# Kernel tuning notes

Measured on AMD Instinct MI355X. Metric: run time of the kernel, lower is better.

The kernel has to match this reference:

```python
import jax, jax.numpy as jnp
import numpy as np
import math

D_MODEL = 1024
NUM_HEADS = 16


def setup_inputs() -> dict:
    key = jax.random.key(0)
    kx, kq, kk, kv, ko = jax.random.split(key, 5)
    std = math.sqrt(2.0 / (D_MODEL + D_MODEL))
    def w(k):
        return (jax.random.truncated_normal(k, -3.0, 3.0, (D_MODEL, D_MODEL), jnp.float32) * std)
    return {
        "x": jax.random.normal(kx, (2, 2048, D_MODEL), jnp.float32),
        "Wq": w(kq),
        "Wk": w(kk),
        "Wv": w(kv),
        "Wo": w(ko),
    }


def reference(x, Wq, Wk, Wv, Wo):
    B, S, D = x.shape
    H = NUM_HEADS
    dh = D // H
    # projections: weight is (d_out, d_in)
    def proj(t, W):
        y = jnp.einsum('bsd,ed->bse', t, W)
        return y.reshape(B, S, H, dh).transpose(0, 2, 1, 3)  # b h s dh
    Q = proj(x, Wq)
    K = proj(x, Wk)
    V = proj(x, Wv)
    scale = 1.0 / math.sqrt(dh)
    logits = jnp.einsum('bhqd,bhkd->bhqk', Q, K) * scale
    mask = jnp.tril(jnp.ones((S, S), dtype=bool))  # causal
    logits = jnp.where(mask, logits, -jnp.inf)
    weights = jax.nn.softmax(logits, axis=-1)
    attn = jnp.einsum('bhqk,bhkd->bhqd', weights, V)
    attn = attn.transpose(0, 2, 1, 3).reshape(B, S, D)
    return jnp.einsum('bsd,ed->bse', attn, Wo)
```

## Files before the change

kernel.cpp:

```cpp
#include <hip/hip_runtime.h>
#include <hip/hip_bf16.h>

typedef __bf16 bf16x8 __attribute__((ext_vector_type(8)));
typedef float  f32x4  __attribute__((ext_vector_type(4)));
typedef float  f32x16 __attribute__((ext_vector_type(16)));
typedef unsigned short u16x8 __attribute__((ext_vector_type(8)));
typedef unsigned short u16x4 __attribute__((ext_vector_type(4)));
typedef unsigned int   u32x4 __attribute__((ext_vector_type(4)));

#define WAITV(N) asm volatile("s_waitcnt vmcnt(" #N ")" ::: "memory")
#define SBAR()   do { __builtin_amdgcn_s_barrier(); asm volatile("" ::: "memory"); } while (0)


__device__ __forceinline__ unsigned short f2bf(float f) {
  return __builtin_bit_cast(unsigned short, (__bf16)f);
}

__device__ __forceinline__ bf16x8 ld8(const unsigned short* p) {
  return __builtin_bit_cast(bf16x8, *reinterpret_cast<const u16x8*>(p));
}

__device__ __forceinline__ unsigned int cvtpk(float a, float b) {
  unsigned int r;
  asm("v_cvt_pk_bf16_f32 %0, %1, %2" : "=v"(r) : "v"(a), "v"(b));
  return r;
}

__device__ __forceinline__ float e2(float x) {
  float r;
  asm("v_exp_f32 %0, %1" : "=v"(r) : "v"(x));
  return r;
}

__device__ __forceinline__ void gload16(const unsigned short* src, unsigned short* lds) {
  __builtin_amdgcn_global_load_lds(
      (const __attribute__((address_space(1))) unsigned int*)src,
      (__attribute__((address_space(3))) unsigned int*)lds,
      16, 0, 0);
}


__global__ __launch_bounds__(256) void cvt_inputs(
    const float* __restrict__ x, const float* __restrict__ Wq,
    const float* __restrict__ Wk, const float* __restrict__ Wv,
    const float* __restrict__ Wo,
    unsigned short* __restrict__ xb, unsigned short* __restrict__ wb) {
  const int NXC = 4194304 / 8;
  const int NWC = 1048576 / 8;
  const int total = NXC + 4 * NWC;
  for (int cid = blockIdx.x * 256 + threadIdx.x; cid < total; cid += gridDim.x * 256) {
    const float* s; unsigned short* d; int off;
    if (cid < NXC) { s = x; d = xb; off = cid * 8; }
    else {
      const int c2 = cid - NXC; const int w = c2 >> 17; const int o2 = c2 & (NWC - 1);
      s = (w == 0) ? Wq : (w == 1) ? Wk : (w == 2) ? Wv : Wo;
      d = wb + (size_t)w * 1048576;
      off = o2 * 8;
    }
    const f32x4 a  = *reinterpret_cast<const f32x4*>(s + off);
    const f32x4 b2 = *reinterpret_cast<const f32x4*>(s + off + 4);
    u16x8 o;
#pragma unroll
    for (int j = 0; j < 4; ++j) { o[j] = f2bf(a[j]); o[j + 4] = f2bf(b2[j]); }
    *reinterpret_cast<u16x8*>(d + off) = o;
  }
}


__global__ __launch_bounds__(256, 2) void gemm_qkv(
    const unsigned short* __restrict__ xb,
    const unsigned short* __restrict__ wb,
    unsigned short* __restrict__ q_s,
    unsigned short* __restrict__ k_s,
    unsigned short* __restrict__ vt_s) {
  __shared__ unsigned short As[2][128 * 64];
  __shared__ unsigned short Bs[2][3][64 * 64];
  const int tid  = threadIdx.x;
  const int lane = tid & 63;
  const int g    = lane >> 4;
  const int lo   = lane & 15;
  const int wid  = tid >> 6;
  const int m0   = blockIdx.y * 128;
  const int n0   = blockIdx.x * 64;
  const int wm   = wid >> 1, wn = wid & 1;

  f32x4 acc[3][4][2] = {};

  auto stage = [&](int buf, int k0) {
#pragma unroll
    for (int i = 0; i < 4; ++i) {
      const int c   = i * 256 + tid;
      const int row = c >> 3, cc = c & 7;
      const int scc = cc ^ (row & 7);
      gload16(xb + (size_t)(m0 + row) * 1024 + k0 + scc * 8, &As[buf][(i * 4 + wid) * 512]);
    }
#pragma unroll
    for (int w = 0; w < 3; ++w)
#pragma unroll
      for (int i = 0; i < 2; ++i) {
        const int c   = i * 256 + tid;
        const int row = c >> 3, cc = c & 7;
        const int scc = cc ^ (row & 7);
        gload16(wb + (size_t)w * 1048576 + (size_t)(n0 + row) * 1024 + k0 + scc * 8,
                &Bs[buf][w][(i * 4 + wid) * 512]);
      }
  };

  stage(0, 0);
  stage(1, 64);
  int cur = 0;
  for (int t = 0; t < 16; ++t) {
    if (t < 15) WAITV(10); else WAITV(0);
    SBAR();
#pragma unroll
    for (int ks = 0; ks < 2; ++ks) {
      const int slot = (ks * 4 + g) ^ (lo & 7);
      bf16x8 af[4];
#pragma unroll
      for (int mi = 0; mi < 4; ++mi)
        af[mi] = ld8(&As[cur][(wm * 64 + mi * 16 + lo) * 64 + slot * 8]);
#pragma unroll
      for (int w = 0; w < 3; ++w) {
        bf16x8 bvf[2];
#pragma unroll
        for (int ni = 0; ni < 2; ++ni)
          bvf[ni] = ld8(&Bs[cur][w][(wn * 32 + ni * 16 + lo) * 64 + slot * 8]);
#pragma unroll
        for (int mi = 0; mi < 4; ++mi)
#pragma unroll
          for (int ni = 0; ni < 2; ++ni)
            acc[w][mi][ni] = __builtin_amdgcn_mfma_f32_16x16x32_bf16(af[mi], bvf[ni], acc[w][mi][ni], 0, 0, 0);
      }
    }
    SBAR();
    if (t + 2 < 16) stage(cur, (t + 2) * 64);
    cur ^= 1;
  }

#pragma unroll
  for (int w = 0; w < 3; ++w) {
    unsigned short* Cv = (w == 0) ? q_s : (w == 1) ? k_s : vt_s;
#pragma unroll
    for (int mi = 0; mi < 4; ++mi) {
#pragma unroll
      for (int ni = 0; ni < 2; ++ni) {
        const int gcol = n0 + wn * 32 + ni * 16 + lo;
        const int h = gcol >> 6, d = gcol & 63;
        if (w == 2) {
          const int s0 = m0 + wm * 64 + mi * 16 + g * 4;
          const int b = s0 >> 11, s = s0 & 2047;
          u16x4 pk;
#pragma unroll
          for (int r = 0; r < 4; ++r) pk[r] = f2bf(acc[w][mi][ni][r]);
          *reinterpret_cast<u16x4*>(&Cv[(((size_t)(b * 16 + h)) * 64 + d) * 2048 + s]) = pk;
        } else {
#pragma unroll
          for (int r = 0; r < 4; ++r) {
            const int grow = m0 + wm * 64 + mi * 16 + g * 4 + r;
            const int b = grow >> 11, s = grow & 2047;
            Cv[(((size_t)(b * 16 + h)) * 2048 + s) * 64 + d] = f2bf(acc[w][mi][ni][r]);
          }
        }
      }
    }
  }
}


__global__ __launch_bounds__(256) void gemm_out(
    const unsigned short* __restrict__ A,
    const unsigned short* __restrict__ wb,
    float* __restrict__ out) {
  const unsigned short* W = wb + (size_t)3 * 1048576;
  __shared__ unsigned short As[2][128 * 64];
  __shared__ unsigned short Bs[2][64 * 64];
  const int tid  = threadIdx.x;
  const int lane = tid & 63;
  const int g    = lane >> 4;
  const int lo   = lane & 15;
  const int wid  = tid >> 6;
  const int m0   = blockIdx.y * 128;
  const int n0   = blockIdx.x * 64;
  const int wm   = wid >> 1, wn = wid & 1;

  f32x4 acc[4][2] = {};

  auto stage = [&](int buf, int k0) {
#pragma unroll
    for (int i = 0; i < 4; ++i) {
      const int c   = i * 256 + tid;
      const int row = c >> 3, cc = c & 7;
      const int scc = cc ^ (row & 7);
      gload16(A + (size_t)(m0 + row) * 1024 + k0 + scc * 8, &As[buf][(i * 4 + wid) * 512]);
    }
#pragma unroll
    for (int i = 0; i < 2; ++i) {
      const int c   = i * 256 + tid;
      const int row = c >> 3, cc = c & 7;
      const int scc = cc ^ (row & 7);
      gload16(W + (size_t)(n0 + row) * 1024 + k0 + scc * 8, &Bs[buf][(i * 4 + wid) * 512]);
    }
  };

  stage(0, 0);
  stage(1, 64);
  int cur = 0;
  for (int t = 0; t < 16; ++t) {
    if (t < 15) WAITV(6); else WAITV(0);
    SBAR();
#pragma unroll
    for (int ks = 0; ks < 2; ++ks) {
      const int slot = (ks * 4 + g) ^ (lo & 7);
      bf16x8 af[4], bvf[2];
#pragma unroll
      for (int mi = 0; mi < 4; ++mi)
        af[mi] = ld8(&As[cur][(wm * 64 + mi * 16 + lo) * 64 + slot * 8]);
#pragma unroll
      for (int ni = 0; ni < 2; ++ni)
        bvf[ni] = ld8(&Bs[cur][(wn * 32 + ni * 16 + lo) * 64 + slot * 8]);
#pragma unroll
      for (int mi = 0; mi < 4; ++mi)
#pragma unroll
        for (int ni = 0; ni < 2; ++ni)
          acc[mi][ni] = __builtin_amdgcn_mfma_f32_16x16x32_bf16(af[mi], bvf[ni], acc[mi][ni], 0, 0, 0);
    }
    SBAR();
    if (t + 2 < 16) stage(cur, (t + 2) * 64);
    cur ^= 1;
  }

#pragma unroll
  for (int mi = 0; mi < 4; ++mi)
#pragma unroll
    for (int ni = 0; ni < 2; ++ni) {
      const int gcol = n0 + wn * 32 + ni * 16 + lo;
#pragma unroll
      for (int r = 0; r < 4; ++r) {
        const int grow = m0 + wm * 64 + mi * 16 + g * 4 + r;
        out[(size_t)grow * 1024 + gcol] = acc[mi][ni][r];
      }
    }
}


__global__ __launch_bounds__(512, 4) void attn_fwd(
    const unsigned short* __restrict__ Q,
    const unsigned short* __restrict__ K,
    const unsigned short* __restrict__ Vt,
    unsigned short* __restrict__ O) {
  __shared__ unsigned short Kl[2][128 * 64];
  __shared__ unsigned short Vl[2][2][64 * 64];
  const int tid  = threadIdx.x;
  const int lane = tid & 63;
  const int wid  = tid >> 6;
  const int qs   = wid & 3;
  const int kh   = wid >> 2;
  const int q31  = lane & 31;
  const int hi   = lane >> 5;
  const int bi   = blockIdx.x;
  const int bh   = bi & 31;
  const int j    = (bi < 256) ? (15 - (bi >> 5)) : ((bi - 256) >> 5);
  const int b    = bh >> 4, h = bh & 15;

  const unsigned short* Qb = Q  + (size_t)bh * 2048 * 64;
  const unsigned short* Kb = K  + (size_t)bh * 2048 * 64;
  const unsigned short* Vb = Vt + (size_t)bh * 64 * 2048;
  const float SC = 0.125f * 1.4426950408889634f;

  auto stage = [&](int buf, int t) {
#pragma unroll
    for (int i = 0; i < 2; ++i) {
      const int c   = i * 512 + tid;
      const int row = c >> 3, cc = c & 7;
      const int scc = cc ^ (row & 7);
      gload16(Kb + (size_t)(t * 128 + row) * 64 + scc * 8, &Kl[buf][(i * 8 + wid) * 512]);
    }
#pragma unroll
    for (int i = 0; i < 2; ++i) {
      const int d  = tid >> 3, cc = tid & 7;
      const int scc = cc ^ (d & 7);
      gload16(Vb + (size_t)d * 2048 + t * 128 + i * 64 + scc * 8, &Vl[buf][i][wid * 512]);
    }
  };

  const int R  = j + 1;
  const int qv = j * 128 + qs * 32 + q31;

  bf16x8 qf[4];
#pragma unroll
  for (int ds = 0; ds < 4; ++ds) {
    bf16x8 tq = ld8(Qb + (size_t)qv * 64 + ds * 16 + hi * 8);
#pragma unroll
    for (int jx = 0; jx < 8; ++jx) tq[jx] = (__bf16)((float)tq[jx] * SC);
    qf[ds] = tq;
  }

  f32x16 oacc[2] = {};
  float m = -1.0e30f;
  float l = 0.f;

  stage(0, 0);
  int buf = 0;

  for (int t = 0; t < R; ++t) {
    SBAR();
    if (t + 1 < R) { stage(buf ^ 1, t + 1); WAITV(4); }
    else WAITV(0);
    SBAR();

    const bool lastt = (t == j);
    const bool skipw = lastt && (kh == 1) && (qs < 2);
    if (!skipw) {
      f32x16 sv[2];
      __builtin_amdgcn_s_setprio(1);
#pragma unroll
      for (int kt2 = 0; kt2 < 2; ++kt2) {
        const int row = kh * 64 + kt2 * 32 + q31;
        f32x16 a = {};
#pragma unroll
        for (int ds = 0; ds < 4; ++ds) {
          bf16x8 kf = ld8(&Kl[buf][row * 64 + ((ds * 2 + hi) ^ (row & 7)) * 8]);
          a = __builtin_amdgcn_mfma_f32_32x32x16_bf16(kf, qf[ds], a, 0, 0, 0);
        }
        sv[kt2] = a;
      }
      __builtin_amdgcn_s_setprio(0);

      const bool domask = lastt && !(kh == 0 && qs >= 2);
      float t0 = -1.0e30f, t1 = -1.0e30f, t2 = -1.0e30f, t3 = -1.0e30f;
      if (domask) {
#pragma unroll
        for (int kt2 = 0; kt2 < 2; ++kt2)
#pragma unroll
          for (int r = 0; r < 16; ++r) {
            float v = sv[kt2][r];
            const int key = t * 128 + kh * 64 + kt2 * 32 + (r & 3) + 8 * (r >> 2) + 4 * hi;
            if (key > qv) v = -INFINITY;
            sv[kt2][r] = v;
            if ((r & 3) == 0) t0 = fmaxf(t0, v);
            else if ((r & 3) == 1) t1 = fmaxf(t1, v);
            else if ((r & 3) == 2) t2 = fmaxf(t2, v);
            else t3 = fmaxf(t3, v);
          }
      } else {
#pragma unroll
        for (int kt2 = 0; kt2 < 2; ++kt2)
#pragma unroll
          for (int r = 0; r < 16; ++r) {
            const float v = sv[kt2][r];
            if ((r & 3) == 0) t0 = fmaxf(t0, v);
            else if ((r & 3) == 1) t1 = fmaxf(t1, v);
            else if ((r & 3) == 2) t2 = fmaxf(t2, v);
            else t3 = fmaxf(t3, v);
          }
      }
      const float tmax = fmaxf(fmaxf(t0, t1), fmaxf(t2, t3));

      if (!__all(tmax <= m + 8.f)) {
        float rmax = fmaxf(tmax, __shfl_xor(tmax, 32));
        const float mn   = fmaxf(m, rmax);
        const float corr = e2(m - mn);
        l *= corr;
#pragma unroll
        for (int dt = 0; dt < 2; ++dt)
#pragma unroll
          for (int r = 0; r < 16; ++r) oacc[dt][r] *= corr;
        m = mn;
      }

      float p0 = 0.f, p1 = 0.f, p2 = 0.f, p3 = 0.f;
#pragma unroll
      for (int kt2 = 0; kt2 < 2; ++kt2)
#pragma unroll
        for (int r = 0; r < 16; ++r) {
          const float p = e2(sv[kt2][r] - m);
          sv[kt2][r] = p;
          if ((r & 3) == 0) p0 += p;
          else if ((r & 3) == 1) p1 += p;
          else if ((r & 3) == 2) p2 += p;
          else p3 += p;
        }
      l += (p0 + p1) + (p2 + p3);

      unsigned int pw[4][4];
#pragma unroll
      for (int ks = 0; ks < 4; ++ks) {
        const int kt2 = ks >> 1, Rr = (ks & 1) * 8;
        unsigned int a0 = cvtpk(sv[kt2][Rr + 0], sv[kt2][Rr + 1]);
        unsigned int c0 = cvtpk(sv[kt2][Rr + 4], sv[kt2][Rr + 5]);
        unsigned int a1 = cvtpk(sv[kt2][Rr + 2], sv[kt2][Rr + 3]);
        unsigned int c1 = cvtpk(sv[kt2][Rr + 6], sv[kt2][Rr + 7]);
        asm("v_permlane32_swap_b32 %0, %1" : "+v"(a0), "+v"(c0));
        asm("v_permlane32_swap_b32 %0, %1" : "+v"(a1), "+v"(c1));
        pw[ks][0] = a0; pw[ks][1] = a1; pw[ks][2] = c0; pw[ks][3] = c1;
      }

      __builtin_amdgcn_s_setprio(1);
#pragma unroll
      for (int dt = 0; dt < 2; ++dt) {
        const int dl = dt * 32 + q31;
#pragma unroll
        for (int ks = 0; ks < 4; ++ks) {
          bf16x8 vfr = ld8(&Vl[buf][kh][dl * 64 + ((ks * 2 + hi) ^ (dl & 7)) * 8]);
          u32x4 t4 = {pw[ks][0], pw[ks][1], pw[ks][2], pw[ks][3]};
          bf16x8 pb = __builtin_bit_cast(bf16x8, t4);
          oacc[dt] = __builtin_amdgcn_mfma_f32_32x32x16_bf16(vfr, pb, oacc[dt], 0, 0, 0);
        }
      }
      __builtin_amdgcn_s_setprio(0);
    }

    buf ^= 1;
  }

  SBAR();
  float* VlF = (float*)&Vl[0][0][0];
  float* KlF = (float*)&Kl[0][0];
  const int mi = qs * 64 + lane;
  if (kh == 1) {
    *reinterpret_cast<f32x16*>(&VlF[mi * 32])      = oacc[0];
    *reinterpret_cast<f32x16*>(&VlF[mi * 32 + 16]) = oacc[1];
    KlF[mi * 2] = m; KlF[mi * 2 + 1] = l;
  }
  SBAR();
  if (kh == 0) {
    const f32x16 o1a = *reinterpret_cast<const f32x16*>(&VlF[mi * 32]);
    const f32x16 o1b = *reinterpret_cast<const f32x16*>(&VlF[mi * 32 + 16]);
    const float m1 = KlF[mi * 2], l1 = KlF[mi * 2 + 1];
    const float mm = fmaxf(m, m1);
    const float c0 = e2(m - mm), c1 = e2(m1 - mm);
    float lr = l * c0 + l1 * c1;
    lr += __shfl_xor(lr, 32);
    const float inv = 1.f / lr;
    const size_t obase = ((size_t)(b * 2048 + qv)) * 1024 + h * 64;
#pragma unroll
    for (int dt = 0; dt < 2; ++dt)
#pragma unroll
      for (int r4 = 0; r4 < 4; ++r4) {
        u16x4 pk;
#pragma unroll
        for (int e = 0; e < 4; ++e) {
          const int r = r4 * 4 + e;
          const float o1 = (dt == 0) ? o1a[r] : o1b[r];
          pk[e] = f2bf((oacc[dt][r] * c0 + o1 * c1) * inv);
        }
        *reinterpret_cast<u16x4*>(&O[obase + dt * 32 + r4 * 8 + hi * 4]) = pk;
      }
  }
}


extern "C" void kernel_launch(void* const* d_in, const int* in_sizes, int n_in,
                              void* d_out, int out_size, void* d_ws, size_t ws_size,
                              hipStream_t stream) {
  const float* x  = (const float*)d_in[0];
  const float* Wq = (const float*)d_in[1];
  const float* Wk = (const float*)d_in[2];
  const float* Wv = (const float*)d_in[3];
  const float* Wo = (const float*)d_in[4];
  float* out = (float*)d_out;

  char* ws = (char*)d_ws;
  const size_t MiB = 1024 * 1024;
  unsigned short* x_bf = (unsigned short*)(ws);
  unsigned short* a_s  = (unsigned short*)(ws);
  unsigned short* w_bf = (unsigned short*)(ws + 8  * MiB);
  unsigned short* q_s  = (unsigned short*)(ws + 16 * MiB);
  unsigned short* k_s  = (unsigned short*)(ws + 24 * MiB);
  unsigned short* vt_s = (unsigned short*)(ws + 32 * MiB);

  cvt_inputs<<<2048, dim3(256), 0, stream>>>(x, Wq, Wk, Wv, Wo, x_bf, w_bf);
  gemm_qkv<<<dim3(16, 32), dim3(256), 0, stream>>>(x_bf, w_bf, q_s, k_s, vt_s);
  attn_fwd<<<512, dim3(512), 0, stream>>>(q_s, k_s, vt_s, a_s);
  gemm_out<<<dim3(16, 32), dim3(256), 0, stream>>>(a_s, w_bf, out);
}
```

Baseline: 89.38 us.

## Fuse fp32-to-bf16 conversion of x into QKV GEMM A-tile staging

```diff
diff --git a/kernel.cpp b/kernel.cpp
--- a/kernel.cpp
+++ b/kernel.cpp
@@ -9,6 +9,7 @@
 typedef unsigned int   u32x4 __attribute__((ext_vector_type(4)));
 
 #define WAITV(N) asm volatile("s_waitcnt vmcnt(" #N ")" ::: "memory")
+#define WAITLG() asm volatile("s_waitcnt lgkmcnt(0)" ::: "memory")
 #define SBAR()   do { __builtin_amdgcn_s_barrier(); asm volatile("" ::: "memory"); } while (0)
 
 
@@ -41,22 +42,16 @@
 
 
 __global__ __launch_bounds__(256) void cvt_inputs(
-    const float* __restrict__ x, const float* __restrict__ Wq,
-    const float* __restrict__ Wk, const float* __restrict__ Wv,
-    const float* __restrict__ Wo,
-    unsigned short* __restrict__ xb, unsigned short* __restrict__ wb) {
-  const int NXC = 4194304 / 8;
+    const float* __restrict__ Wq, const float* __restrict__ Wk,
+    const float* __restrict__ Wv, const float* __restrict__ Wo,
+    unsigned short* __restrict__ wb) {
   const int NWC = 1048576 / 8;
-  const int total = NXC + 4 * NWC;
+  const int total = 4 * NWC;
   for (int cid = blockIdx.x * 256 + threadIdx.x; cid < total; cid += gridDim.x * 256) {
-    const float* s; unsigned short* d; int off;
-    if (cid < NXC) { s = x; d = xb; off = cid * 8; }
-    else {
-      const int c2 = cid - NXC; const int w = c2 >> 17; const int o2 = c2 & (NWC - 1);
-      s = (w == 0) ? Wq : (w == 1) ? Wk : (w == 2) ? Wv : Wo;
-      d = wb + (size_t)w * 1048576;
-      off = o2 * 8;
-    }
+    const int w = cid >> 17; const int o2 = cid & (NWC - 1);
+    const float* s = (w == 0) ? Wq : (w == 1) ? Wk : (w == 2) ? Wv : Wo;
+    unsigned short* d = wb + (size_t)w * 1048576;
+    const int off = o2 * 8;
     const f32x4 a  = *reinterpret_cast<const f32x4*>(s + off);
     const f32x4 b2 = *reinterpret_cast<const f32x4*>(s + off + 4);
     u16x8 o;
@@ -68,7 +63,7 @@
 
 
 __global__ __launch_bounds__(256, 2) void gemm_qkv(
-    const unsigned short* __restrict__ xb,
+    const float* __restrict__ xf,
     const unsigned short* __restrict__ wb,
     unsigned short* __restrict__ q_s,
     unsigned short* __restrict__ k_s,
@@ -85,15 +80,33 @@
   const int wm   = wid >> 1, wn = wid & 1;
 
   f32x4 acc[3][4][2] = {};
-
-  auto stage = [&](int buf, int k0) {
+  f32x4 rA[8];
+
+  auto issueA = [&](int k0) {
 #pragma unroll
     for (int i = 0; i < 4; ++i) {
       const int c   = i * 256 + tid;
       const int row = c >> 3, cc = c & 7;
       const int scc = cc ^ (row & 7);
-      gload16(xb + (size_t)(m0 + row) * 1024 + k0 + scc * 8, &As[buf][(i * 4 + wid) * 512]);
-    }
+      const float* src = xf + (size_t)(m0 + row) * 1024 + k0 + scc * 8;
+      rA[2 * i]     = *reinterpret_cast<const f32x4*>(src);
+      rA[2 * i + 1] = *reinterpret_cast<const f32x4*>(src + 4);
+    }
+  };
+  auto writeA = [&](int buf) {
+#pragma unroll
+    for (int i = 0; i < 4; ++i) {
+      const int c = i * 256 + tid;
+      u16x8 o;
+#pragma unroll
+      for (int jx = 0; jx < 4; ++jx) {
+        o[jx]     = f2bf(rA[2 * i][jx]);
+        o[jx + 4] = f2bf(rA[2 * i + 1][jx]);
+      }
+      *reinterpret_cast<u16x8*>(&As[buf][c * 8]) = o;
+    }
+  };
+  auto issueB = [&](int buf, int k0) {
 #pragma unroll
     for (int w = 0; w < 3; ++w)
 #pragma unroll
@@ -106,12 +119,14 @@
       }
   };
 
-  stage(0, 0);
-  stage(1, 64);
+  issueA(0);  WAITV(0); writeA(0); issueB(0, 0);
+  issueA(64); WAITV(0); writeA(1); issueB(1, 64);
+  WAITLG();
+
   int cur = 0;
   for (int t = 0; t < 16; ++t) {
-    if (t < 15) WAITV(10); else WAITV(0);
-    SBAR();
+    SBAR();
+    if (t + 2 < 16) issueA((t + 2) * 64);
 #pragma unroll
     for (int ks = 0; ks < 2; ++ks) {
       const int slot = (ks * 4 + g) ^ (lo & 7);
@@ -133,7 +148,14 @@
       }
     }
     SBAR();
-    if (t + 2 < 16) stage(cur, (t + 2) * 64);
+    if (t + 2 < 16) {
+      WAITV(0);
+      writeA(cur);
+      issueB(cur, (t + 2) * 64);
+      WAITLG();
+    } else if (t + 1 < 16) {
+      WAITV(0);
+    }
     cur ^= 1;
   }
 
@@ -462,15 +484,14 @@
 
   char* ws = (char*)d_ws;
   const size_t MiB = 1024 * 1024;
-  unsigned short* x_bf = (unsigned short*)(ws);
   unsigned short* a_s  = (unsigned short*)(ws);
   unsigned short* w_bf = (unsigned short*)(ws + 8  * MiB);
   unsigned short* q_s  = (unsigned short*)(ws + 16 * MiB);
   unsigned short* k_s  = (unsigned short*)(ws + 24 * MiB);
   unsigned short* vt_s = (unsigned short*)(ws + 32 * MiB);
 
-  cvt_inputs<<<2048, dim3(256), 0, stream>>>(x, Wq, Wk, Wv, Wo, x_bf, w_bf);
-  gemm_qkv<<<dim3(16, 32), dim3(256), 0, stream>>>(x_bf, w_bf, q_s, k_s, vt_s);
+  cvt_inputs<<<2048, dim3(256), 0, stream>>>(Wq, Wk, Wv, Wo, w_bf);
+  gemm_qkv<<<dim3(16, 32), dim3(256), 0, stream>>>(x, w_bf, q_s, k_s, vt_s);
   attn_fwd<<<512, dim3(512), 0, stream>>>(q_s, k_s, vt_s, a_s);
   gemm_out<<<dim3(16, 32), dim3(256), 0, stream>>>(a_s, w_bf, out);
 }
```

Result: slower. 99.94 us (+11.8%).
